# Kernel tuning notes

Hardware: AMD Instinct MI355X
Metric: run time of the kernel (lower is better)

Reference implementation:

```python
import jax, jax.numpy as jnp
import numpy as np

NF = 64            # n_filter
CFAC = 3           # SinSobel c_factor: identity + sobel-x + sobel-y
FIN = NF * CFAC    # dyna block input channels (192)
FH = NF * 2        # dyna hidden (128)
FOUT = NF          # dyna output (64)
LAT = 512
N_CALLS = 6        # ceil(log2(128) - log2(2))
P_SIZES = [FH * FIN, FH, FH * FH, FH, FOUT * FH, FOUT, FOUT * FIN, FOUT]
P_TOTAL = sum(P_SIZES)  # 61824
_OFFS = np.cumsum([0] + P_SIZES)

def act(t):
    return jax.nn.leaky_relu(t, 0.2)

def conv1x1(x, w, b):
    # x [B,I,H,W], w [O,I] -> [B,O,H,W]
    return jnp.einsum('bihw,oi->bohw', x, w) + b[None, :, None, None]

def res_block(x, w0, b0, w1, b1):
    # GAN-stability style residual block with 1x1 convs
    return x + 0.1 * conv1x1(act(conv1x1(act(x), w0, b0)), w1, b1)

def depthwise3x3(x, k2d):
    C = x.shape[1]
    k = jnp.broadcast_to(k2d.astype(x.dtype), (C, 1, 3, 3))
    return jax.lax.conv_general_dilated(
        x, k, (1, 1), [(1, 1), (1, 1)],
        dimension_numbers=('NCHW', 'OIHW', 'NCHW'),
        feature_group_count=C)

SOBEL_X = jnp.array([[1., 0., -1.], [2., 0., -2.], [1., 0., -1.]], jnp.float32) / 8.0
SOBEL_Y = SOBEL_X.T
_g = jnp.exp(-0.5 * jnp.array([-1., 0., 1.], jnp.float32) ** 2)
GAUSS = jnp.outer(_g, _g)
GAUSS = GAUSS / GAUSS.sum()

def sin_sobel(x):
    return jnp.concatenate([x, depthwise3x3(x, SOBEL_X), depthwise3x3(x, SOBEL_Y)], axis=1)

def dyna_residual(x, params):
    # per-sample hypernetwork-generated 1x1-conv residual block
    B = x.shape[0]
    def take(i, shape):
        return params[:, _OFFS[i]:_OFFS[i + 1]].reshape((B,) + shape)
    w_in, b_in = take(0, (FH, FIN)), take(1, (FH,))
    w_mid, b_mid = take(2, (FH, FH)), take(3, (FH,))
    w_out, b_out = take(4, (FOUT, FH)), take(5, (FOUT,))
    w_sk, b_sk = take(6, (FOUT, FIN)), take(7, (FOUT,))
    def pconv(h, w, b):  # batched per-sample 1x1 conv
        return jnp.einsum('bihw,boi->bohw', h, w) + b[:, :, None, None]
    x_s = pconv(x, w_sk, b_sk)
    dx = pconv(x, w_in, b_in)
    dx = pconv(act(dx), w_mid, b_mid)
    dx = pconv(act(dx), w_out, b_out)
    return x_s + dx

def downsample(x):
    # GaussianSmoothing(k=3, sigma=1, pad=1) then bilinear 0.5
    # (align_corners=False bilinear at scale 0.5 == 2x2 average pooling)
    x = depthwise3x3(x, GAUSS)
    B, C, H, W = x.shape
    return x.reshape(B, C, H // 2, 2, W // 2, 2).mean(axis=(3, 5))

def lin_res(x, w1, b1, w2, b2, sw=None, sb=None):
    x_s = x if sw is None else x @ sw + sb
    return x_s + 0.1 * (act(act(x) @ w1 + b1) @ w2 + b2)

def forward(x, inj_lat, leak, in_w, in_b, inrb_w0, inrb_b0, inrb_w1, inrb_b1,
            hyp_w, hyp_b, outrb_w0, outrb_b0, outrb_w1, outrb_b1,
            l1_sw, l1_sb, l1_w1, l1_b1, l1_w2, l1_b2,
            l2_w1, l2_b1, l2_w2, l2_b2, lo_w, lo_b):
    out = conv1x1(x, in_w, in_b)
    out = res_block(out, inrb_w0, inrb_b0, inrb_w1, inrb_b1)
    leak_f = jnp.clip(leak, 0.001, 1000.0)
    dyn_params = inj_lat @ hyp_w + hyp_b  # [B, P_TOTAL], shared across calls
    out_embs = [out]
    for _ in range(N_CALLS):  # fixed small layer loop; spatial dims halve each call
        out_new = sin_sobel(out)
        out_new = dyna_residual(out_new, dyn_params)
        out = out + leak_f * out_new
        out = downsample(out)
        out_embs.append(out)
    out = res_block(out, outrb_w0, outrb_b0, outrb_w1, outrb_b1)
    h = out.mean(axis=(2, 3))  # [B, NF]
    h = lin_res(h, l1_w1, l1_b1, l1_w2, l1_b2, l1_sw, l1_sb)
    h = lin_res(h, l2_w1, l2_b1, l2_w2, l2_b2)
    lat = h @ lo_w + lo_b
    return lat, out_embs

def setup_inputs() -> dict:
    key = jax.random.key(0)
    ks = jax.random.split(key, 24)
    B, C, S = 8, 3, 128
    def rn(k, shape, scale=0.05):
        return scale * jax.random.normal(k, shape, jnp.float32)
    z = lambda n: jnp.zeros((n,), jnp.float32)
    return {
        'x': jax.random.normal(ks[0], (B, C, S, S), jnp.float32),
        'inj_lat': jax.random.normal(ks[1], (B, LAT), jnp.float32),
        'leak': jnp.array(0.1, jnp.float32),
        'in_w': rn(ks[2], (NF, C)), 'in_b': z(NF),
        'inrb_w0': rn(ks[3], (NF, NF)), 'inrb_b0': z(NF),
        'inrb_w1': rn(ks[4], (NF, NF)), 'inrb_b1': z(NF),
        'hyp_w': rn(ks[5], (LAT, P_TOTAL), 0.01), 'hyp_b': rn(ks[6], (P_TOTAL,), 0.01),
        'outrb_w0': rn(ks[7], (NF, NF)), 'outrb_b0': z(NF),
        'outrb_w1': rn(ks[8], (NF, NF)), 'outrb_b1': z(NF),
        'l1_sw': rn(ks[9], (NF, LAT)), 'l1_sb': z(LAT),
        'l1_w1': rn(ks[10], (NF, 2 * LAT)), 'l1_b1': z(2 * LAT),
        'l1_w2': rn(ks[11], (2 * LAT, LAT)), 'l1_b2': z(LAT),
        'l2_w1': rn(ks[12], (LAT, LAT)), 'l2_b1': z(LAT),
        'l2_w2': rn(ks[13], (LAT, LAT)), 'l2_b2': z(LAT),
        'lo_w': rn(ks[14], (LAT, LAT)), 'lo_b': z(LAT),
    }

def reference(x, inj_lat, leak, in_w, in_b, inrb_w0, inrb_b0, inrb_w1, inrb_b1,
              hyp_w, hyp_b, outrb_w0, outrb_b0, outrb_w1, outrb_b1,
              l1_sw, l1_sb, l1_w1, l1_b1, l1_w2, l1_b2,
              l2_w1, l2_b1, l2_w2, l2_b2, lo_w, lo_b):
    lat, out_embs = forward(x, inj_lat, leak, in_w, in_b, inrb_w0, inrb_b0, inrb_w1, inrb_b1,
                            hyp_w, hyp_b, outrb_w0, outrb_b0, outrb_w1, outrb_b1,
                            l1_sw, l1_sb, l1_w1, l1_b1, l1_w2, l1_b2,
                            l2_w1, l2_b1, l2_w2, l2_b2, lo_w, lo_b)
    return (lat, *out_embs)
```

## Files before the change

### kernel.cpp

```cpp
#include <hip/hip_runtime.h>


#define BATCH 8
#define PT 61824

typedef __attribute__((ext_vector_type(8))) short bf16x8;
typedef __attribute__((ext_vector_type(4))) float f32x4;

__device__ __forceinline__ float lrelu(float v) { return v > 0.f ? v : 0.2f * v; }

__device__ __forceinline__ short f2bf(float f) {
    union { float fv; unsigned u; } v; v.fv = f;
    return (short)((v.u + 0x7fffu + ((v.u >> 16) & 1u)) >> 16);
}

__global__ __launch_bounds__(256) void hyper_kernel(
    const float* __restrict__ inj, const float* __restrict__ hw,
    const float* __restrict__ hb, float* __restrict__ dyn,
    short* __restrict__ dyn16)
{
    __shared__ float s_l[512 * 8];
    int t = threadIdx.x;
    for (int i = t; i < 4096; i += 256) {
        int b = i >> 9, k = i & 511;
        s_l[k * 8 + b] = inj[i];
    }
    __syncthreads();
    int p = blockIdx.x * 256 + t;
    if (p >= PT) return;
    float acc[8];
#pragma unroll
    for (int b = 0; b < 8; ++b) acc[b] = 0.f;
    for (int k = 0; k < 512; ++k) {
        float w = hw[(size_t)k * PT + p];
        float4 a0 = *(const float4*)&s_l[k * 8];
        float4 a1 = *(const float4*)&s_l[k * 8 + 4];
        acc[0] += a0.x * w; acc[1] += a0.y * w; acc[2] += a0.z * w; acc[3] += a0.w * w;
        acc[4] += a1.x * w; acc[5] += a1.y * w; acc[6] += a1.z * w; acc[7] += a1.w * w;
    }
    float bias = hb[p];
#pragma unroll
    for (int b = 0; b < 8; ++b) {
        float v = acc[b] + bias;
        dyn[(size_t)b * PT + p] = v;
        dyn16[(size_t)b * PT + p] = f2bf(v);
    }
}

__global__ __launch_bounds__(256) void stem_kernel(
    const float* __restrict__ x, const float* __restrict__ in_w,
    const float* __restrict__ in_b,
    const float* __restrict__ w0, const float* __restrict__ b0,
    const float* __restrict__ w1, const float* __restrict__ b1,
    float* __restrict__ out0)
{
    const int HW = 128 * 128;
    __shared__ float s_t0[64 * 68];
    __shared__ short s_vh[2 * 64 * 72];
    __shared__ float s_x[192];
    short* s_v = s_vh;
    short* s_h = s_vh + 64 * 72;
    float* s_y = (float*)s_vh;

    const int b = blockIdx.x >> 8;
    const int tile = blockIdx.x & 255;
    const int pix0 = tile * 64;
    const int t = threadIdx.x;
    const int l = t & 63, w = t >> 6;
    const int lp = l & 15, lq = l >> 4;

    if (t < 192) s_x[t] = x[(size_t)b * 3 * HW + (t >> 6) * HW + pix0 + (t & 63)];
    __syncthreads();

    for (int j = t; j < 1024; j += 256) {
        int p = j & 63, cg = j >> 6;
        float x0 = s_x[p], x1 = s_x[64 + p], x2 = s_x[128 + p];
        short pk[4];
#pragma unroll
        for (int cc = 0; cc < 4; ++cc) {
            int c = cg * 4 + cc;
            float v = in_b[c] + x0 * in_w[c * 3] + x1 * in_w[c * 3 + 1]
                    + x2 * in_w[c * 3 + 2];
            s_t0[c * 68 + p] = v;
            pk[cc] = f2bf(lrelu(v));
        }
        *(short4*)&s_v[p * 72 + cg * 4] = make_short4(pk[0], pk[1], pk[2], pk[3]);
    }
    __syncthreads();

    const int o = w * 16 + lp;
    const f32x4 z4 = {0.f, 0.f, 0.f, 0.f};

    bf16x8 wb0[2], wb1[2];
#pragma unroll
    for (int k = 0; k < 2; ++k) {
        bf16x8 p0, p1;
#pragma unroll
        for (int e = 0; e < 8; ++e) {
            p0[e] = f2bf(w0[o * 64 + k * 32 + lq * 8 + e]);
            p1[e] = f2bf(w1[o * 64 + k * 32 + lq * 8 + e]);
        }
        wb0[k] = p0; wb1[k] = p1;
    }

    {
        f32x4 acc[4];
#pragma unroll
        for (int mt = 0; mt < 4; ++mt) acc[mt] = z4;
#pragma unroll
        for (int k = 0; k < 2; ++k)
#pragma unroll
            for (int mt = 0; mt < 4; ++mt) {
                bf16x8 a = *(const bf16x8*)&s_v[(mt * 16 + lp) * 72 + k * 32 + lq * 8];
                acc[mt] = __builtin_amdgcn_mfma_f32_16x16x32_bf16(a, wb0[k], acc[mt], 0, 0, 0);
            }
        float bi = b0[o];
#pragma unroll
        for (int mt = 0; mt < 4; ++mt)
#pragma unroll
            for (int r = 0; r < 4; ++r)
                s_h[(mt * 16 + lq * 4 + r) * 72 + o] = f2bf(lrelu(acc[mt][r] + bi));
    }
    __syncthreads();

    {
        f32x4 acc[4];
#pragma unroll
        for (int mt = 0; mt < 4; ++mt) acc[mt] = z4;
#pragma unroll
        for (int k = 0; k < 2; ++k)
#pragma unroll
            for (int mt = 0; mt < 4; ++mt) {
                bf16x8 a = *(const bf16x8*)&s_h[(mt * 16 + lp) * 72 + k * 32 + lq * 8];
                acc[mt] = __builtin_amdgcn_mfma_f32_16x16x32_bf16(a, wb1[k], acc[mt], 0, 0, 0);
            }
        float bi = b1[o];
        __syncthreads();
#pragma unroll
        for (int mt = 0; mt < 4; ++mt) {
            f32x4 dv;
#pragma unroll
            for (int r = 0; r < 4; ++r) dv[r] = 0.1f * (acc[mt][r] + bi);
            *(f32x4*)&s_y[o * 68 + mt * 16 + lq * 4] = dv;
        }
    }
    __syncthreads();

#pragma unroll
    for (int v = 0; v < 4; ++v) {
        int idx = v * 1024 + t * 4;
        int oo = idx >> 6, px = idx & 63;
        f32x4 t0v = *(const f32x4*)&s_t0[oo * 68 + px];
        f32x4 dv = *(const f32x4*)&s_y[oo * 68 + px];
        f32x4 ov = t0v + dv;
        *(f32x4*)&out0[((size_t)b * 64 + oo) * HW + pix0 + px] = ov;
    }
}

template<int MT>
__global__ __launch_bounds__(256) void iter_kernel(
    const float* __restrict__ cur, const float* __restrict__ dynf,
    const short* __restrict__ dynb, const float* __restrict__ leak_p,
    float* __restrict__ y, int S, int sh)
{
    constexpr int PX = MT * 16;
    constexpr int SY = (MT == 4) ? 68 : 20;
    __shared__ short s_s[PX * 200];
    __shared__ short s_h[PX * 136];
    float* s_y = (float*)s_s;

    const int HW = S * S;
    const int tilesPer = HW / PX;
    const int b = blockIdx.x / tilesPer;
    const int tile = blockIdx.x - b * tilesPer;
    const int pix0 = tile * PX;
    const int t = threadIdx.x;
    const int l = t & 63, w = t >> 6;
    const int lp = l & 15, lq = l >> 4;
    const float* base = cur + (size_t)b * 64 * HW;

    {
        const int p = (MT == 4) ? (lp + 16 * w) : lp;
        const int gpx = pix0 + p;
        const int row = gpx >> sh;
        const int x = gpx & (S - 1);
        const bool rm = (row > 0), rp = (row < S - 1);
        const bool le = (lp == 0) && (x > 0);
        const bool re = (lp == 15) && (x < S - 1);
        const int iters = (MT == 4) ? 8 : 2;
        int* s32 = (int*)s_s;
        for (int i = 0; i < iters; ++i) {
            const int cp = (MT == 4) ? (lq + 4 * i) : (lq + 4 * w + 16 * i);
            unsigned pk_id = 0, pk_sx = 0, pk_sy = 0;
#pragma unroll
            for (int cc = 0; cc < 2; ++cc) {
                const int c = 2 * cp + cc;
                const float* ch = base + (size_t)c * HW + row * S;
                float vm = rm ? ch[x - S] : 0.f;
                float v0 = ch[x];
                float vp = rp ? ch[x + S] : 0.f;
                float elm = 0.f, el0 = 0.f, elp = 0.f, erm = 0.f, er0 = 0.f, erp = 0.f;
                if (le) { elm = rm ? ch[x - 1 - S] : 0.f; el0 = ch[x - 1]; elp = rp ? ch[x - 1 + S] : 0.f; }
                if (re) { erm = rm ? ch[x + 1 - S] : 0.f; er0 = ch[x + 1]; erp = rp ? ch[x + 1 + S] : 0.f; }
                float Lm = __shfl(vm, l - 1), L0 = __shfl(v0, l - 1), Lp = __shfl(vp, l - 1);
                float Rm = __shfl(vm, l + 1), R0 = __shfl(v0, l + 1), Rp = __shfl(vp, l + 1);
                if (lp == 0)  { Lm = elm; L0 = el0; Lp = elp; }
                if (lp == 15) { Rm = erm; R0 = er0; Rp = erp; }
                if (x == 0)     { Lm = 0.f; L0 = 0.f; Lp = 0.f; }
                if (x == S - 1) { Rm = 0.f; R0 = 0.f; Rp = 0.f; }
                float sx = (Lm - Rm + 2.f * (L0 - R0) + Lp - Rp) * 0.125f;
                float sy = (Lm + 2.f * vm + Rm - Lp - 2.f * vp - Rp) * 0.125f;
                unsigned hid = (unsigned short)f2bf(v0);
                unsigned hsx = (unsigned short)f2bf(sx);
                unsigned hsy = (unsigned short)f2bf(sy);
                pk_id |= hid << (16 * cc);
                pk_sx |= hsx << (16 * cc);
                pk_sy |= hsy << (16 * cc);
            }
            s32[p * 100 + cp] = (int)pk_id;
            s32[p * 100 + 32 + cp] = (int)pk_sx;
            s32[p * 100 + 64 + cp] = (int)pk_sy;
        }
    }
    __syncthreads();

    const short* wb = dynb + (size_t)b * PT;
    const float* pf = dynf + (size_t)b * PT;
    const f32x4 z4 = {0.f, 0.f, 0.f, 0.f};

    {
        f32x4 acc[2][MT];
#pragma unroll
        for (int n = 0; n < 2; ++n)
#pragma unroll
            for (int mt = 0; mt < MT; ++mt) acc[n][mt] = z4;
        for (int k = 0; k < 6; ++k) {
            bf16x8 a[MT];
#pragma unroll
            for (int mt = 0; mt < MT; ++mt)
                a[mt] = *(const bf16x8*)&s_s[(mt * 16 + lp) * 200 + k * 32 + lq * 8];
#pragma unroll
            for (int n = 0; n < 2; ++n) {
                int o = (w * 2 + n) * 16 + lp;
                bf16x8 bb = *(const bf16x8*)&wb[o * 192 + k * 32 + lq * 8];
#pragma unroll
                for (int mt = 0; mt < MT; ++mt)
                    acc[n][mt] = __builtin_amdgcn_mfma_f32_16x16x32_bf16(a[mt], bb, acc[n][mt], 0, 0, 0);
            }
        }
#pragma unroll
        for (int n = 0; n < 2; ++n) {
            int o = (w * 2 + n) * 16 + lp;
            float bi = pf[24576 + o];
#pragma unroll
            for (int mt = 0; mt < MT; ++mt)
#pragma unroll
                for (int r = 0; r < 4; ++r)
                    s_h[(mt * 16 + lq * 4 + r) * 136 + o] = f2bf(lrelu(acc[n][mt][r] + bi));
        }
    }
    __syncthreads();

    {
        f32x4 acc[2][MT];
#pragma unroll
        for (int n = 0; n < 2; ++n)
#pragma unroll
            for (int mt = 0; mt < MT; ++mt) acc[n][mt] = z4;
        for (int k = 0; k < 4; ++k) {
            bf16x8 a[MT];
#pragma unroll
            for (int mt = 0; mt < MT; ++mt)
                a[mt] = *(const bf16x8*)&s_h[(mt * 16 + lp) * 136 + k * 32 + lq * 8];
#pragma unroll
            for (int n = 0; n < 2; ++n) {
                int o = (w * 2 + n) * 16 + lp;
                bf16x8 bb = *(const bf16x8*)&wb[24704 + o * 128 + k * 32 + lq * 8];
#pragma unroll
                for (int mt = 0; mt < MT; ++mt)
                    acc[n][mt] = __builtin_amdgcn_mfma_f32_16x16x32_bf16(a[mt], bb, acc[n][mt], 0, 0, 0);
            }
        }
        __syncthreads();
#pragma unroll
        for (int n = 0; n < 2; ++n) {
            int o = (w * 2 + n) * 16 + lp;
            float bi = pf[41088 + o];
#pragma unroll
            for (int mt = 0; mt < MT; ++mt)
#pragma unroll
                for (int r = 0; r < 4; ++r)
                    s_h[(mt * 16 + lq * 4 + r) * 136 + o] = f2bf(lrelu(acc[n][mt][r] + bi));
        }
    }
    __syncthreads();

    {
        f32x4 acc[MT];
#pragma unroll
        for (int mt = 0; mt < MT; ++mt) acc[mt] = z4;
        int o = w * 16 + lp;
        for (int k = 0; k < 4; ++k) {
            bf16x8 bb = *(const bf16x8*)&wb[41216 + o * 128 + k * 32 + lq * 8];
#pragma unroll
            for (int mt = 0; mt < MT; ++mt) {
                bf16x8 a = *(const bf16x8*)&s_h[(mt * 16 + lp) * 136 + k * 32 + lq * 8];
                acc[mt] = __builtin_amdgcn_mfma_f32_16x16x32_bf16(a, bb, acc[mt], 0, 0, 0);
            }
        }
        for (int k = 0; k < 6; ++k) {
            bf16x8 bb = *(const bf16x8*)&wb[49472 + o * 192 + k * 32 + lq * 8];
#pragma unroll
            for (int mt = 0; mt < MT; ++mt) {
                bf16x8 a = *(const bf16x8*)&s_s[(mt * 16 + lp) * 200 + k * 32 + lq * 8];
                acc[mt] = __builtin_amdgcn_mfma_f32_16x16x32_bf16(a, bb, acc[mt], 0, 0, 0);
            }
        }
        float bi = pf[49408 + o] + pf[61760 + o];
        __syncthreads();
#pragma unroll
        for (int mt = 0; mt < MT; ++mt)
#pragma unroll
            for (int r = 0; r < 4; ++r)
                s_y[o * SY + mt * 16 + lq * 4 + r] = acc[mt][r] + bi;
    }
    __syncthreads();

    {
        float lk = fminf(fmaxf(leak_p[0], 0.001f), 1000.f);
        if (MT == 4) {
#pragma unroll
            for (int v = 0; v < 4; ++v) {
                int idx = v * 1024 + t * 4;
                int o = idx >> 6, px = idx & 63;
                f32x4 sv = *(const f32x4*)&s_y[o * SY + px];
                const float* cb = cur + ((size_t)b * 64 + o) * HW + pix0 + px;
                float* yb = y + ((size_t)b * 64 + o) * HW + pix0 + px;
                f32x4 cv = *(const f32x4*)cb;
                *(f32x4*)yb = cv + lk * sv;
            }
        } else {
            int o = t >> 2, px = (t & 3) * 4;
            f32x4 sv = *(const f32x4*)&s_y[o * SY + px];
            const float* cb = cur + ((size_t)b * 64 + o) * HW + pix0 + px;
            float* yb = y + ((size_t)b * 64 + o) * HW + pix0 + px;
            f32x4 cv = *(const f32x4*)cb;
            *(f32x4*)yb = cv + lk * sv;
        }
    }
}

__global__ __launch_bounds__(256) void down_kernel(
    const float* __restrict__ yin, float* __restrict__ outp, int S, int total)
{
    int idx = blockIdx.x * 256 + threadIdx.x;
    if (idx >= total) return;
    const float ga = 0.60653065971263342f;
    const float gs = 1.f / ((1.f + 2.f * ga) * (1.f + 2.f * ga));
    float g1[3] = {ga, 1.f, ga};
    int S2 = S >> 1;
    int ox = idx % S2;
    int r = idx / S2;
    int oy = r % S2;
    int bc = r / S2;
    const float* src = yin + (size_t)bc * S * S;
    float acc = 0.f;
#pragma unroll
    for (int py = 0; py < 2; ++py)
#pragma unroll
        for (int px = 0; px < 2; ++px) {
            int cy = 2 * oy + py, cx = 2 * ox + px;
#pragma unroll
            for (int dy = 0; dy < 3; ++dy) {
                int ay = cy + dy - 1;
                if (ay < 0 || ay >= S) continue;
#pragma unroll
                for (int dx = 0; dx < 3; ++dx) {
                    int ax = cx + dx - 1;
                    if (ax < 0 || ax >= S) continue;
                    acc += g1[dy] * g1[dx] * src[ay * S + ax];
                }
            }
        }
    outp[idx] = acc * 0.25f * gs;
}

__global__ __launch_bounds__(256) void head_a_kernel(
    const float* __restrict__ emb6,
    const float* __restrict__ w0, const float* __restrict__ b0,
    const float* __restrict__ w1, const float* __restrict__ b1,
    float* __restrict__ h)
{
    __shared__ float sm_t[256], sm_v[256], sm_r[256];
    int b = blockIdx.x, t = threadIdx.x;
    sm_t[t] = emb6[b * 256 + t];
    __syncthreads();
    {
        int o = t & 63, p = t >> 6;
        float acc = 0.f;
        for (int k = 0; k < 64; ++k) acc += w0[o * 64 + k] * lrelu(sm_t[k * 4 + p]);
        sm_v[o * 4 + p] = lrelu(acc + b0[o]);
    }
    __syncthreads();
    {
        int o = t & 63, p = t >> 6;
        float acc = 0.f;
        for (int k = 0; k < 64; ++k) acc += w1[o * 64 + k] * sm_v[k * 4 + p];
        sm_r[o * 4 + p] = sm_t[o * 4 + p] + 0.1f * (acc + b1[o]);
    }
    __syncthreads();
    if (t < 64)
        h[b * 64 + t] = 0.25f * (sm_r[t * 4] + sm_r[t * 4 + 1] + sm_r[t * 4 + 2] + sm_r[t * 4 + 3]);
}

__global__ __launch_bounds__(256) void head_b_kernel(
    const float* __restrict__ h, const float* __restrict__ w,
    const float* __restrict__ bias, float* __restrict__ t1)
{
    __shared__ float s_h[64];
    int id = blockIdx.x * 256 + threadIdx.x;
    int b = id >> 10, o = id & 1023;
    if (threadIdx.x < 64) s_h[threadIdx.x] = lrelu(h[b * 64 + threadIdx.x]);
    __syncthreads();
    float acc = 0.f;
    for (int k = 0; k < 64; ++k) acc += s_h[k] * w[k * 1024 + o];
    t1[b * 1024 + o] = lrelu(acc + bias[o]);
}

__global__ __launch_bounds__(256) void head_c_kernel(
    const float* __restrict__ h, const float* __restrict__ t1,
    const float* __restrict__ sw, const float* __restrict__ sb,
    const float* __restrict__ w2, const float* __restrict__ b2,
    float* __restrict__ h1)
{
    __shared__ float s_t[8 * 128];
    __shared__ float s_h[8 * 64];
    int oblk = blockIdx.x & 1, chunk = blockIdx.x >> 1;
    int t = threadIdx.x;
    int o = oblk * 256 + t;
    for (int j = t; j < 1024; j += 256) {
        int b = j >> 7, kk = j & 127;
        s_t[j] = t1[b * 1024 + chunk * 128 + kk];
    }
    if (chunk == 0)
        for (int j = t; j < 512; j += 256) s_h[j] = h[j];
    __syncthreads();
    float acc[8];
#pragma unroll
    for (int b = 0; b < 8; ++b) acc[b] = 0.f;
    for (int kk = 0; kk < 128; ++kk) {
        float wv = w2[(chunk * 128 + kk) * 512 + o];
#pragma unroll
        for (int b = 0; b < 8; ++b) acc[b] += s_t[b * 128 + kk] * wv;
    }
#pragma unroll
    for (int b = 0; b < 8; ++b) acc[b] *= 0.1f;
    if (chunk == 0) {
        for (int k = 0; k < 64; ++k) {
            float wv = sw[k * 512 + o];
#pragma unroll
            for (int b = 0; b < 8; ++b) acc[b] += s_h[b * 64 + k] * wv;
        }
        float c0 = sb[o] + 0.1f * b2[o];
#pragma unroll
        for (int b = 0; b < 8; ++b) acc[b] += c0;
    }
#pragma unroll
    for (int b = 0; b < 8; ++b) atomicAdd(&h1[b * 512 + o], acc[b]);
}

__global__ __launch_bounds__(256) void head_d_kernel(
    const float* __restrict__ h1, const float* __restrict__ w,
    const float* __restrict__ bias, float* __restrict__ z3)
{
    __shared__ float s_u[8 * 64];
    int oblk = blockIdx.x & 1, chunk = blockIdx.x >> 1;
    int t = threadIdx.x;
    int o = oblk * 256 + t;
    for (int j = t; j < 512; j += 256) {
        int b = j >> 6, kk = j & 63;
        s_u[j] = lrelu(h1[b * 512 + chunk * 64 + kk]);
    }
    __syncthreads();
    float acc[8];
#pragma unroll
    for (int b = 0; b < 8; ++b) acc[b] = 0.f;
    for (int kk = 0; kk < 64; ++kk) {
        float wv = w[(chunk * 64 + kk) * 512 + o];
#pragma unroll
        for (int b = 0; b < 8; ++b) acc[b] += s_u[b * 64 + kk] * wv;
    }
    if (chunk == 0) {
        float c0 = bias[o];
#pragma unroll
        for (int b = 0; b < 8; ++b) acc[b] += c0;
    }
#pragma unroll
    for (int b = 0; b < 8; ++b) atomicAdd(&z3[b * 512 + o], acc[b]);
}

__global__ __launch_bounds__(256) void head_e_kernel(
    const float* __restrict__ h1, const float* __restrict__ z3,
    const float* __restrict__ w, const float* __restrict__ bias,
    float* __restrict__ h2)
{
    __shared__ float s_u[8 * 64];
    int oblk = blockIdx.x & 1, chunk = blockIdx.x >> 1;
    int t = threadIdx.x;
    int o = oblk * 256 + t;
    for (int j = t; j < 512; j += 256) {
        int b = j >> 6, kk = j & 63;
        s_u[j] = lrelu(z3[b * 512 + chunk * 64 + kk]);
    }
    __syncthreads();
    float acc[8];
#pragma unroll
    for (int b = 0; b < 8; ++b) acc[b] = 0.f;
    for (int kk = 0; kk < 64; ++kk) {
        float wv = w[(chunk * 64 + kk) * 512 + o];
#pragma unroll
        for (int b = 0; b < 8; ++b) acc[b] += s_u[b * 64 + kk] * wv;
    }
#pragma unroll
    for (int b = 0; b < 8; ++b) acc[b] *= 0.1f;
    if (chunk == 0) {
        float c0 = 0.1f * bias[o];
#pragma unroll
        for (int b = 0; b < 8; ++b) acc[b] += h1[b * 512 + o] + c0;
    }
#pragma unroll
    for (int b = 0; b < 8; ++b) atomicAdd(&h2[b * 512 + o], acc[b]);
}

__global__ __launch_bounds__(256) void head_f_kernel(
    const float* __restrict__ h2, const float* __restrict__ w,
    const float* __restrict__ bias, float* __restrict__ lat)
{
    __shared__ float s_u[8 * 64];
    int oblk = blockIdx.x & 1, chunk = blockIdx.x >> 1;
    int t = threadIdx.x;
    int o = oblk * 256 + t;
    for (int j = t; j < 512; j += 256) {
        int b = j >> 6, kk = j & 63;
        s_u[j] = h2[b * 512 + chunk * 64 + kk];
    }
    __syncthreads();
    float acc[8];
#pragma unroll
    for (int b = 0; b < 8; ++b) acc[b] = 0.f;
    for (int kk = 0; kk < 64; ++kk) {
        float wv = w[(chunk * 64 + kk) * 512 + o];
#pragma unroll
        for (int b = 0; b < 8; ++b) acc[b] += s_u[b * 64 + kk] * wv;
    }
    if (chunk == 0) {
        float c0 = bias[o];
#pragma unroll
        for (int b = 0; b < 8; ++b) acc[b] += c0;
    }
#pragma unroll
    for (int b = 0; b < 8; ++b) atomicAdd(&lat[b * 512 + o], acc[b]);
}

extern "C" void kernel_launch(void* const* d_in, const int* in_sizes, int n_in,
                              void* d_out, int out_size, void* d_ws, size_t ws_size,
                              hipStream_t stream) {
    const float* x      = (const float*)d_in[0];
    const float* inj    = (const float*)d_in[1];
    const float* leak   = (const float*)d_in[2];
    const float* in_w   = (const float*)d_in[3];
    const float* in_b   = (const float*)d_in[4];
    const float* inrb_w0 = (const float*)d_in[5];
    const float* inrb_b0 = (const float*)d_in[6];
    const float* inrb_w1 = (const float*)d_in[7];
    const float* inrb_b1 = (const float*)d_in[8];
    const float* hyp_w  = (const float*)d_in[9];
    const float* hyp_b  = (const float*)d_in[10];
    const float* outrb_w0 = (const float*)d_in[11];
    const float* outrb_b0 = (const float*)d_in[12];
    const float* outrb_w1 = (const float*)d_in[13];
    const float* outrb_b1 = (const float*)d_in[14];
    const float* l1_sw  = (const float*)d_in[15];
    const float* l1_sb  = (const float*)d_in[16];
    const float* l1_w1  = (const float*)d_in[17];
    const float* l1_b1  = (const float*)d_in[18];
    const float* l1_w2  = (const float*)d_in[19];
    const float* l1_b2  = (const float*)d_in[20];
    const float* l2_w1  = (const float*)d_in[21];
    const float* l2_b1  = (const float*)d_in[22];
    const float* l2_w2  = (const float*)d_in[23];
    const float* l2_b2  = (const float*)d_in[24];
    const float* lo_w   = (const float*)d_in[25];
    const float* lo_b   = (const float*)d_in[26];

    float* out = (float*)d_out;
    float* dyn = (float*)d_ws;
    float* ybuf = dyn + (size_t)BATCH * PT;
    short* dyn16 = (short*)(ybuf + (size_t)BATCH * 64 * 16384);
    float* hbuf = (float*)(dyn16 + (size_t)BATCH * PT);
    float* t1buf = hbuf + 512;
    float* h1buf = t1buf + 8192;
    float* z3buf = h1buf + 4096;
    float* h2buf = z3buf + 4096;

    hipMemsetAsync(h1buf, 0, (4096 * 3) * sizeof(float), stream);
    hipMemsetAsync(out, 0, 4096 * sizeof(float), stream);

    hyper_kernel<<<(PT + 255) / 256, 256, 0, stream>>>(inj, hyp_w, hyp_b, dyn, dyn16);

    size_t cur = 4096;
    stem_kernel<<<BATCH * 256, 256, 0, stream>>>(
        x, in_w, in_b, inrb_w0, inrb_b0, inrb_w1, inrb_b1, out + cur);

    int S = 128, sh = 7;
    for (int i = 0; i < 6; ++i) {
        if (S >= 64) {
            iter_kernel<4><<<BATCH * (S * S / 64), 256, 0, stream>>>(
                out + cur, dyn, dyn16, leak, ybuf, S, sh);
        } else {
            iter_kernel<1><<<BATCH * (S * S / 16), 256, 0, stream>>>(
                out + cur, dyn, dyn16, leak, ybuf, S, sh);
        }
        int S2 = S >> 1;
        int total = BATCH * 64 * S2 * S2;
        size_t nxt = cur + (size_t)BATCH * 64 * S * S;
        down_kernel<<<(total + 255) / 256, 256, 0, stream>>>(ybuf, out + nxt, S, total);
        cur = nxt;
        S = S2; sh -= 1;
    }

    head_a_kernel<<<BATCH, 256, 0, stream>>>(
        out + cur, outrb_w0, outrb_b0, outrb_w1, outrb_b1, hbuf);
    head_b_kernel<<<32, 256, 0, stream>>>(hbuf, l1_w1, l1_b1, t1buf);
    head_c_kernel<<<16, 256, 0, stream>>>(hbuf, t1buf, l1_sw, l1_sb, l1_w2, l1_b2, h1buf);
    head_d_kernel<<<16, 256, 0, stream>>>(h1buf, l2_w1, l2_b1, z3buf);
    head_e_kernel<<<16, 256, 0, stream>>>(h1buf, z3buf, l2_w2, l2_b2, h2buf);
    head_f_kernel<<<16, 256, 0, stream>>>(h2buf, lo_w, lo_b, out);
}
```

Before: 534.3 us.

## Fuse skip GEMM into first dyna GEMM and tile separable downsample in LDS

The skip-path 1x1 conv MFMAs now run inside the first hidden GEMM loop, reusing the already-loaded perception A fragments. The result is carried as the initial accumulator of the output GEMM, so the second pass over s_s and one barrier are gone. The downsample kernel is rewritten to stage an input tile in shared memory and apply the Gaussian-plus-average as two separable 4-tap passes. This replaces the 36 guarded global loads per output. The trade-off is extra register pressure from the carried skip accumulators, plus shared-memory staging and barriers in the downsample.

```diff
diff --git a/kernel.cpp b/kernel.cpp
--- a/kernel.cpp
+++ b/kernel.cpp
@@ -228,12 +228,17 @@
     const float* pf = dynf + (size_t)b * PT;
     const f32x4 z4 = {0.f, 0.f, 0.f, 0.f};
 
+    f32x4 acc_sk[MT];
+#pragma unroll
+    for (int mt = 0; mt < MT; ++mt) acc_sk[mt] = z4;
+
     {
         f32x4 acc[2][MT];
 #pragma unroll
         for (int n = 0; n < 2; ++n)
 #pragma unroll
             for (int mt = 0; mt < MT; ++mt) acc[n][mt] = z4;
+        const int osk = w * 16 + lp;
         for (int k = 0; k < 6; ++k) {
             bf16x8 a[MT];
 #pragma unroll
@@ -247,6 +252,12 @@
                 for (int mt = 0; mt < MT; ++mt)
                     acc[n][mt] = __builtin_amdgcn_mfma_f32_16x16x32_bf16(a[mt], bb, acc[n][mt], 0, 0, 0);
             }
+            {
+                bf16x8 bsk = *(const bf16x8*)&wb[49472 + osk * 192 + k * 32 + lq * 8];
+#pragma unroll
+                for (int mt = 0; mt < MT; ++mt)
+                    acc_sk[mt] = __builtin_amdgcn_mfma_f32_16x16x32_bf16(a[mt], bsk, acc_sk[mt], 0, 0, 0);
+            }
         }
 #pragma unroll
         for (int n = 0; n < 2; ++n) {
@@ -298,7 +309,7 @@
     {
         f32x4 acc[MT];
 #pragma unroll
-        for (int mt = 0; mt < MT; ++mt) acc[mt] = z4;
+        for (int mt = 0; mt < MT; ++mt) acc[mt] = acc_sk[mt];
         int o = w * 16 + lp;
         for (int k = 0; k < 4; ++k) {
             bf16x8 bb = *(const bf16x8*)&wb[41216 + o * 128 + k * 32 + lq * 8];
@@ -308,16 +319,7 @@
                 acc[mt] = __builtin_amdgcn_mfma_f32_16x16x32_bf16(a, bb, acc[mt], 0, 0, 0);
             }
         }
-        for (int k = 0; k < 6; ++k) {
-            bf16x8 bb = *(const bf16x8*)&wb[49472 + o * 192 + k * 32 + lq * 8];
-#pragma unroll
-            for (int mt = 0; mt < MT; ++mt) {
-                bf16x8 a = *(const bf16x8*)&s_s[(mt * 16 + lp) * 200 + k * 32 + lq * 8];
-                acc[mt] = __builtin_amdgcn_mfma_f32_16x16x32_bf16(a, bb, acc[mt], 0, 0, 0);
-            }
-        }
         float bi = pf[49408 + o] + pf[61760 + o];
-        __syncthreads();
 #pragma unroll
         for (int mt = 0; mt < MT; ++mt)
 #pragma unroll
@@ -351,38 +353,65 @@
 }
 
 __global__ __launch_bounds__(256) void down_kernel(
-    const float* __restrict__ yin, float* __restrict__ outp, int S, int total)
-{
-    int idx = blockIdx.x * 256 + threadIdx.x;
-    if (idx >= total) return;
+    const float* __restrict__ yin, float* __restrict__ outp,
+    int S, int S2, int TW, int CPB, int tiles)
+{
+    __shared__ float s_in[3072];
+    __shared__ float s_hb[1152];
+
     const float ga = 0.60653065971263342f;
     const float gs = 1.f / ((1.f + 2.f * ga) * (1.f + 2.f * ga));
-    float g1[3] = {ga, 1.f, ga};
-    int S2 = S >> 1;
-    int ox = idx % S2;
-    int r = idx / S2;
-    int oy = r % S2;
-    int bc = r / S2;
-    const float* src = yin + (size_t)bc * S * S;
-    float acc = 0.f;
-#pragma unroll
-    for (int py = 0; py < 2; ++py)
-#pragma unroll
-        for (int px = 0; px < 2; ++px) {
-            int cy = 2 * oy + py, cx = 2 * ox + px;
-#pragma unroll
-            for (int dy = 0; dy < 3; ++dy) {
-                int ay = cy + dy - 1;
-                if (ay < 0 || ay >= S) continue;
-#pragma unroll
-                for (int dx = 0; dx < 3; ++dx) {
-                    int ax = cx + dx - 1;
-                    if (ax < 0 || ax >= S) continue;
-                    acc += g1[dy] * g1[dx] * src[ay * S + ax];
-                }
-            }
-        }
-    outp[idx] = acc * 0.25f * gs;
+    const float u0 = ga, u1 = 1.f + ga;
+
+    const int t = threadIdx.x;
+    const int bi = blockIdx.x;
+    const int tix = bi % tiles;
+    const int rem = bi / tiles;
+    const int tiy = rem % tiles;
+    const int cg = rem / tiles;
+    const int bc0 = cg * CPB;
+
+    const int IH = 2 * TW + 2;
+    const int IW = IH;
+    const int IWP = IW + 2;
+    const int HS = TW + 1;
+    const int gy0 = tiy * 2 * TW - 1;
+    const int gx0 = tix * 2 * TW - 1;
+
+    const int loadTot = CPB * IH * IW;
+    for (int j = t; j < loadTot; j += 256) {
+        int c = j / (IH * IW);
+        int r = j - c * (IH * IW);
+        int iy = r / IW, ix = r - iy * IW;
+        int gy = gy0 + iy, gx = gx0 + ix;
+        float v = 0.f;
+        if (gy >= 0 && gy < S && gx >= 0 && gx < S)
+            v = yin[(size_t)(bc0 + c) * S * S + gy * S + gx];
+        s_in[(c * IH + iy) * IWP + ix] = v;
+    }
+    __syncthreads();
+
+    const int hTot = CPB * IH * TW;
+    for (int j = t; j < hTot; j += 256) {
+        int c = j / (IH * TW);
+        int r = j - c * (IH * TW);
+        int iy = r / TW, ox = r - iy * TW;
+        const float* pin = &s_in[(c * IH + iy) * IWP + 2 * ox];
+        s_hb[(c * IH + iy) * HS + ox] =
+            u0 * (pin[0] + pin[3]) + u1 * (pin[1] + pin[2]);
+    }
+    __syncthreads();
+
+    {
+        int ox = t % TW;
+        int r = t / TW;
+        int oy = r % TW;
+        int c = r / TW;
+        const float* ph = &s_hb[(c * IH + 2 * oy) * HS + ox];
+        float acc = u0 * (ph[0] + ph[3 * HS]) + u1 * (ph[HS] + ph[2 * HS]);
+        outp[(size_t)(bc0 + c) * S2 * S2 + (tiy * TW + oy) * S2 + tix * TW + ox] =
+            acc * 0.25f * gs;
+    }
 }
 
 __global__ __launch_bounds__(256) void head_a_kernel(
@@ -622,9 +651,13 @@
                 out + cur, dyn, dyn16, leak, ybuf, S, sh);
         }
         int S2 = S >> 1;
-        int total = BATCH * 64 * S2 * S2;
         size_t nxt = cur + (size_t)BATCH * 64 * S * S;
-        down_kernel<<<(total + 255) / 256, 256, 0, stream>>>(ybuf, out + nxt, S, total);
+        int TW = (S2 >= 16) ? 16 : S2;
+        int tiles = S2 / TW;
+        int CPB = 256 / (TW * TW);
+        if (CPB < 1) CPB = 1;
+        int grid = (BATCH * 64 / CPB) * tiles * tiles;
+        down_kernel<<<grid, 256, 0, stream>>>(ybuf, out + nxt, S, S2, TW, CPB, tiles);
         cur = nxt;
         S = S2; sh -= 1;
     }
```

After: 529.7 us. No clear change (-0.9%).
